# Performance work log

Measured on AMD Instinct MI355X. Metric: run time of the kernel, lower is better.

The kernel has to match this reference:

```python
import jax, jax.numpy as jnp
import numpy as np
from jax import lax

T, B, I, H, C = 256, 64, 256, 512, 64
TOP_K, TRUNC, EPS = 5, 100, 1e-7


def setup_inputs() -> dict:
    key = jax.random.key(0)
    ks = jax.random.split(key, 8)
    s = 1.0 / np.sqrt(H).astype(np.float32)
    return {
        "x": jax.random.normal(ks[0], (T, B, I), jnp.float32),
        "W_ih": jax.random.uniform(ks[1], (4 * H, I), jnp.float32, -s, s),
        "W_hh": jax.random.uniform(ks[2], (4 * H, H), jnp.float32, -s, s),
        "b_ih": jax.random.uniform(ks[3], (4 * H,), jnp.float32, -s, s),
        "b_hh": jax.random.uniform(ks[4], (4 * H,), jnp.float32, -s, s),
        "w_t": jax.random.normal(ks[5], (2 * H, 1), jnp.float32) * 0.01,
        "fc_w": jax.random.normal(ks[6], (C, 2 * H), jnp.float32) * (1.0 / np.sqrt(2.0 * H)),
        "fc_b": jnp.zeros((C,), jnp.float32),
    }


def _forward(x, W_ih, W_hh, b_ih, b_hh, w_t, fc_w, fc_b):
    Tn, Bn, _ = x.shape
    Hn = W_hh.shape[1]
    h0 = jnp.zeros((Bn, Hn), x.dtype)
    c0 = jnp.zeros((Bn, Hn), x.dtype)
    # fixed-size memory buffer; slot 0 holds initial h (zeros), slot i+1 gets h_t of step i
    mem0 = jnp.zeros((Tn, Bn, Hn), x.dtype)
    idx = jnp.arange(Tn)
    wt_vec = w_t[:, 0]

    def step(carry, inp):
        h, c, mem = carry
        x_t, i = inp
        detach = ((i + 1) % TRUNC) == 0  # truncated BPTT boundary
        h_in = jnp.where(detach, lax.stop_gradient(h), h)
        c_in = jnp.where(detach, lax.stop_gradient(c), c)
        gates = x_t @ W_ih.T + b_ih + h_in @ W_hh.T + b_hh  # [B,4H]
        gi, gf, gg, go = jnp.split(gates, 4, axis=1)
        c_new = jax.nn.sigmoid(gf) * c_in + jax.nn.sigmoid(gi) * jnp.tanh(gg)
        h_new = jax.nn.sigmoid(go) * jnp.tanh(c_new)

        valid = (idx <= i)[:, None]  # [T,1]; cur_mem_size = i+1
        feat = jnp.tanh(jnp.concatenate(
            [jnp.broadcast_to(h_new[None], mem.shape), mem], axis=2))  # [T,B,2H]
        scores = jnp.einsum('tbd,d->tb', feat, wt_vec)  # [T,B]
        # top-k threshold over valid memory slots (k-th largest), else min when mem small
        kth = lax.top_k(jnp.where(valid, scores, -jnp.inf).T, TOP_K)[0][:, -1]  # [B]
        mn = jnp.min(jnp.where(valid, scores, jnp.inf), axis=0)  # [B]
        delta = jnp.where(i + 1 <= TOP_K, mn, kth) + EPS
        w = jnp.where(valid, jnp.maximum(scores - delta[None, :], 0.0), 0.0)
        w = w / (jnp.sum(w, axis=0, keepdims=True) + EPS)
        m_t = jnp.einsum('tb,tbh->bh', w, mem)
        h_out = h_new + m_t
        mem = mem.at[i + 1].set(h_out, mode='drop')  # append; OOB at last step dropped
        return (h_out, c_new, mem), (h_out, m_t)

    _, (h_seq, m_seq) = lax.scan(step, (h0, c0, mem0), (x, idx))
    feats = jnp.concatenate([h_seq, m_seq], axis=2)  # [T,B,2H]
    return jnp.einsum('tbd,cd->tbc', feats, fc_w) + fc_b  # [T,B,C]


def reference(x, W_ih, W_hh, b_ih, b_hh, w_t, fc_w, fc_b):
    return _forward(x, W_ih, W_hh, b_ih, b_hh, w_t, fc_w, fc_b)
```

## Files before the change

kernel.cpp:

```cpp
#include <hip/hip_runtime.h>


#define T_N 256
#define B_N 64
#define I_N 256
#define H_N 512
#define C_N 64
#define EPSF 1e-7f

typedef float v4f __attribute__((ext_vector_type(4)));
typedef float v2f __attribute__((ext_vector_type(2)));

#define XT4_F   0u
#define MEM4_F  4194304u
#define MSEQ4_F 12615680u
#define PSUM4_F 21004288u
#define FCWT_F  25214976u
#define FLAG_F  25280512u
#define TOT_F   25280768u

__device__ __forceinline__ float sigf(float x) { return 1.0f / (1.0f + expf(-x)); }

__device__ __forceinline__ void st_lic_f32(float* p, float v) {
  asm volatile("global_store_dword %0, %1, off sc0 sc1" :: "v"(p), "v"(v) : "memory");
}
__device__ __forceinline__ void st_lic_f32x2(float* p, v2f v) {
  asm volatile("global_store_dwordx2 %0, %1, off sc0 sc1" :: "v"(p), "v"(v) : "memory");
}
__device__ __forceinline__ void st_lic_u32(unsigned* p, unsigned v) {
  asm volatile("global_store_dword %0, %1, off sc0 sc1" :: "v"(p), "v"(v) : "memory");
}
__device__ __forceinline__ unsigned ld_lic_u32(const unsigned* p) {
  unsigned r;
  asm volatile("global_load_dword %0, %1, off sc0 sc1\n\ts_waitcnt vmcnt(0)"
               : "=v"(r) : "v"(p) : "memory");
  return r;
}

__device__ __forceinline__ void ins5(float s, int t,
                                     float& v0, float& v1, float& v2, float& v3, float& v4,
                                     int& j0, int& j1, int& j2, int& j3) {
  if (s > v4) {
    if (s > v0)      { v4=v3; v3=v2; j3=j2; v2=v1; j2=j1; v1=v0; j1=j0; v0=s; j0=t; }
    else if (s > v1) { v4=v3; v3=v2; j3=j2; v2=v1; j2=j1; v1=s; j1=t; }
    else if (s > v2) { v4=v3; v3=v2; j3=j2; v2=s; j2=t; }
    else if (s > v3) { v4=v3; v3=s; j3=t; }
    else             { v4=s; }
  }
}

__global__ void poison_k(float* out, int n) {
  int i = blockIdx.x * 256 + threadIdx.x;
  if (i < n) out[i] = __int_as_float(0x7fc00000);
}

__global__ void init_k(const float* __restrict__ x, const float* __restrict__ fc_w,
                       float* __restrict__ ws) {
  __shared__ float tile[64][65];
  const int blk = blockIdx.x, tid = threadIdx.x;
  if (blk < 1024) {
    const int t = blk >> 2, k0 = (blk & 3) * 64;
    for (int u = tid; u < 4096; u += 256) {
      int bb = u >> 6, kk = u & 63;
      tile[kk][bb] = x[((unsigned)t * 64u + bb) * 256u + k0 + kk];
    }
    __syncthreads();
    for (int u = tid; u < 4096; u += 256) {
      int kk = u >> 6, bb = u & 63;
      int k = k0 + kk;
      ws[XT4_F + (unsigned)t * 16384u + (unsigned)(k >> 2) * 256u
         + (unsigned)bb * 4u + (unsigned)(k & 3)] = tile[kk][bb];
    }
  } else {
    const int d0 = (blk - 1024) * 64;
    for (int u = tid; u < 4096; u += 256) {
      int cc = u >> 6, dd = u & 63;
      tile[dd][cc] = fc_w[(unsigned)cc * 1024u + d0 + dd];
    }
    __syncthreads();
    for (int u = tid; u < 4096; u += 256) {
      int dd = u >> 6, cc = u & 63;
      ws[FCWT_F + (unsigned)(d0 + dd) * 64u + cc] = tile[dd][cc];
    }
  }
}

__launch_bounds__(512, 1)
__global__ void lstm_main(const float* __restrict__ W_ih, const float* __restrict__ W_hh,
                          const float* __restrict__ b_ih, const float* __restrict__ b_hh,
                          const float* __restrict__ w_t, float* __restrict__ ws) {
  __shared__ float Wx[I_N][8];
  __shared__ float Wh[H_N][8];
  __shared__ float red2[8][4][B_N][2];
  __shared__ float psum[8][B_N];

  const int g = blockIdx.x;
  const int tid = threadIdx.x;
  const int b = tid & 63;
  const int kqu = __builtin_amdgcn_readfirstlane(tid >> 6);

  unsigned int* flags = (unsigned int*)(ws + FLAG_F);

  for (int idx = tid; idx < 8 * I_N; idx += 512) {
    int rr = idx >> 8, k = idx & (I_N - 1);
    int grow = (rr >> 1) * H_N + 2 * g + (rr & 1);
    Wx[k][rr] = W_ih[grow * I_N + k];
  }
  for (int idx = tid; idx < 8 * H_N; idx += 512) {
    int rr = idx >> 9, k = idx & (H_N - 1);
    int grow = (rr >> 1) * H_N + 2 * g + (rr & 1);
    Wh[k][rr] = W_hh[grow * H_N + k];
  }
  float bias_r[8];
  #pragma unroll
  for (int r = 0; r < 8; ++r) {
    int grow = (r >> 1) * H_N + 2 * g + (r & 1);
    bias_r[r] = b_ih[grow] + b_hh[grow];
  }
  const float wt20 = w_t[H_N + 2 * g];
  const float wt21 = w_t[H_N + 2 * g + 1];
  __syncthreads();

  float cs0 = 0.0f, cs1 = 0.0f;
  float v0 = -3e38f, v1 = -3e38f, v2 = -3e38f, v3 = -3e38f, v4 = -3e38f;
  int j0 = 0, j1 = 0, j2 = 0, j3 = 0;
  float mn = 3e38f;

  const unsigned hoff0 = (unsigned)(g >> 1) * 256u + (unsigned)b * 4u + (unsigned)((g & 1) * 2);

  float xacc[8];
  #pragma unroll
  for (int r = 0; r < 8; ++r) xacc[r] = 0.0f;
  {
    const v4f* xp = (const v4f*)(ws + XT4_F) + (unsigned)(kqu * 8) * 64u + b;
    v4f xv[8];
    #pragma unroll
    for (int j = 0; j < 8; ++j) xv[j] = xp[j * 64];
    #pragma unroll
    for (int j = 0; j < 8; ++j) {
      #pragma unroll
      for (int u = 0; u < 4; ++u) {
        float v = xv[j][u];
        const float* wr = &Wx[kqu * 32 + 4 * j + u][0];
        #pragma unroll
        for (int r = 0; r < 8; ++r) xacc[r] += v * wr[r];
      }
    }
  }

  for (int i = 0; i < T_N; ++i) {
    if (i > 0) {
      const unsigned* fp = flags + (kqu * 32 + (b & 31));
      while (ld_lic_u32(fp) < (unsigned)i) __builtin_amdgcn_s_sleep(1);
    }

    v4f pv[8];
    {
      const v4f* pp = (const v4f*)(ws + PSUM4_F) + (unsigned)i * 4096u
                      + (unsigned)(kqu * 8) * 64u + b;
      #pragma unroll
      for (int j = 0; j < 8; ++j) pv[j] = pp[j * 64];
    }
    v4f hv[16];
    {
      const v4f* hp = (const v4f*)(ws + MEM4_F) + (unsigned)i * 8192u
                      + (unsigned)(kqu * 16) * 64u + b;
      #pragma unroll
      for (int j = 0; j < 16; ++j) hv[j] = hp[j * 64];
    }
    float ps = 0.0f;
    #pragma unroll
    for (int j = 0; j < 8; ++j) ps += (pv[j][0] + pv[j][1]) + (pv[j][2] + pv[j][3]);
    psum[kqu][b] = ps;

    float acc[8];
    #pragma unroll
    for (int r = 0; r < 8; ++r) acc[r] = xacc[r];
    #pragma unroll
    for (int j = 0; j < 16; ++j) {
      #pragma unroll
      for (int u = 0; u < 4; ++u) {
        float v = hv[j][u];
        const float* wr = &Wh[kqu * 64 + 4 * j + u][0];
        #pragma unroll
        for (int r = 0; r < 8; ++r) acc[r] += v * wr[r];
      }
    }
    #pragma unroll
    for (int p = 0; p < 4; ++p) {
      red2[kqu][p][b][0] = acc[2 * p];
      red2[kqu][p][b][1] = acc[2 * p + 1];
    }
    __syncthreads();

    float sc = ((psum[0][b] + psum[1][b]) + (psum[2][b] + psum[3][b]))
             + ((psum[4][b] + psum[5][b]) + (psum[6][b] + psum[7][b]));
    ins5(sc, i, v0, v1, v2, v3, v4, j0, j1, j2, j3);
    mn = fminf(mn, sc);
    float delta = ((i + 1) <= 5 ? mn : v4) + EPSF;
    float w0 = fmaxf(v0 - delta, 0.0f);
    float w1 = fmaxf(v1 - delta, 0.0f);
    float w2 = fmaxf(v2 - delta, 0.0f);
    float w3 = fmaxf(v3 - delta, 0.0f);
    float inv = 1.0f / (w0 + w1 + w2 + w3 + EPSF);
    w0 *= inv; w1 *= inv; w2 *= inv; w3 *= inv;

    const v2f* mb2 = (const v2f*)(ws + MEM4_F + hoff0);
    v2f q0 = mb2[(unsigned)j0 * 16384u];
    v2f q1 = mb2[(unsigned)j1 * 16384u];
    v2f q2 = mb2[(unsigned)j2 * 16384u];
    v2f q3 = mb2[(unsigned)j3 * 16384u];

    float G[8];
    #pragma unroll
    for (int r = 0; r < 8; ++r) G[r] = bias_r[r];
    #pragma unroll
    for (int q = 0; q < 8; ++q) {
      #pragma unroll
      for (int p = 0; p < 4; ++p) {
        G[2 * p]     += red2[q][p][b][0];
        G[2 * p + 1] += red2[q][p][b][1];
      }
    }

    float cn0 = sigf(G[2]) * cs0 + sigf(G[0]) * tanhf(G[4]);
    float hn0 = sigf(G[6]) * tanhf(cn0);
    float cn1 = sigf(G[3]) * cs1 + sigf(G[1]) * tanhf(G[5]);
    float hn1 = sigf(G[7]) * tanhf(cn1);
    cs0 = cn0; cs1 = cn1;

    float m0 = w0 * q0[0] + w1 * q1[0] + w2 * q2[0] + w3 * q3[0];
    float m1 = w0 * q0[1] + w1 * q1[1] + w2 * q2[1] + w3 * q3[1];
    float ho0 = hn0 + m0, ho1 = hn1 + m1;

    if (kqu == 0) {
      v2f hov; hov[0] = ho0; hov[1] = ho1;
      st_lic_f32x2(ws + MEM4_F + (unsigned)(i + 1) * 32768u + hoff0, hov);
    } else if (kqu == 1) {
      v2f mv; mv[0] = m0; mv[1] = m1;
      *(v2f*)(ws + MSEQ4_F + (unsigned)i * 32768u + hoff0) = mv;
    } else if (kqu == 2) {
      st_lic_f32(ws + PSUM4_F + (unsigned)(i + 1) * 16384u + (unsigned)(g >> 2) * 256u
                 + (unsigned)b * 4u + (unsigned)(g & 3),
                 tanhf(ho0) * wt20 + tanhf(ho1) * wt21);
    }
    __syncthreads();
    if (tid == 0) st_lic_u32(&flags[g], (unsigned)(i + 1));

    if (i + 1 < T_N) {
      const v4f* xp = (const v4f*)(ws + XT4_F) + (unsigned)(i + 1) * 4096u
                      + (unsigned)(kqu * 8) * 64u + b;
      v4f xv[8];
      #pragma unroll
      for (int j = 0; j < 8; ++j) xv[j] = xp[j * 64];
      #pragma unroll
      for (int r = 0; r < 8; ++r) xacc[r] = 0.0f;
      #pragma unroll
      for (int j = 0; j < 8; ++j) {
        #pragma unroll
        for (int u = 0; u < 4; ++u) {
          float v = xv[j][u];
          const float* wr = &Wx[kqu * 32 + 4 * j + u][0];
          #pragma unroll
          for (int r = 0; r < 8; ++r) xacc[r] += v * wr[r];
        }
      }
    }
  }
}

__launch_bounds__(256, 4)
__global__ void out_gemm(const float* __restrict__ ws, const float* __restrict__ fc_b,
                         float* __restrict__ out) {
  __shared__ float fw[64][16];
  const int t = blockIdx.x >> 2, cg = blockIdx.x & 3;
  const int tid = threadIdx.x, b = tid & 63, cs = (tid >> 6) * 4;
  float acc[4] = {0.0f, 0.0f, 0.0f, 0.0f};
  const v4f* hsrc = (const v4f*)(ws + MEM4_F) + (unsigned)(t + 1) * 8192u + b;
  const v4f* msrc = (const v4f*)(ws + MSEQ4_F) + (unsigned)t * 8192u + b;
  for (int half = 0; half < 2; ++half) {
    const v4f* src = half ? msrc : hsrc;
    for (int dt = 0; dt < 512; dt += 64) {
      __syncthreads();
      for (int u = tid; u < 1024; u += 256) {
        int dd = u >> 4, cc = u & 15;
        fw[dd][cc] = ws[FCWT_F + (unsigned)(half * 512 + dt + dd) * 64u + cg * 16 + cc];
      }
      __syncthreads();
      #pragma unroll 4
      for (int j = 0; j < 16; ++j) {
        v4f f4 = src[(unsigned)(dt / 4 + j) * 64u];
        #pragma unroll
        for (int u = 0; u < 4; ++u) {
          float f = f4[u];
          const float* wr = &fw[4 * j + u][cs];
          #pragma unroll
          for (int c4 = 0; c4 < 4; ++c4) acc[c4] += f * wr[c4];
        }
      }
    }
  }
  float* op = out + ((unsigned)t * 64u + b) * 64u + cg * 16 + cs;
  #pragma unroll
  for (int c4 = 0; c4 < 4; ++c4) op[c4] = acc[c4] + fc_b[cg * 16 + cs + c4];
}

extern "C" void kernel_launch(void* const* d_in, const int* in_sizes, int n_in,
                              void* d_out, int out_size, void* d_ws, size_t ws_size,
                              hipStream_t stream) {
  const float* x    = (const float*)d_in[0];
  const float* W_ih = (const float*)d_in[1];
  const float* W_hh = (const float*)d_in[2];
  const float* b_ih = (const float*)d_in[3];
  const float* b_hh = (const float*)d_in[4];
  const float* w_t  = (const float*)d_in[5];
  const float* fc_w = (const float*)d_in[6];
  const float* fc_b = (const float*)d_in[7];
  float* out = (float*)d_out;
  float* ws  = (float*)d_ws;

  if (ws_size < (size_t)TOT_F * 4u) {
    poison_k<<<(out_size + 255) / 256, 256, 0, stream>>>(out, out_size);
    return;
  }

  hipMemsetAsync(ws + MEM4_F, 0, (size_t)32768u * 4u, stream);
  hipMemsetAsync(ws + PSUM4_F, 0, (size_t)16384u * 4u, stream);
  hipMemsetAsync(ws + FLAG_F, 0, 256u * 4u, stream);

  init_k<<<1040, 256, 0, stream>>>(x, fc_w, ws);
  lstm_main<<<256, 512, 0, stream>>>(W_ih, W_hh, b_ih, b_hh, w_t, ws);
  out_gemm<<<1024, 256, 0, stream>>>(ws, fc_b, out);
}
```

Before: 1.692 ms.

## Remove second block barrier per step via double-buffered LDS and per-wave flags

Double-buffers the shared reduction arrays by step parity so the trailing __syncthreads can be dropped. Each of two waves now publishes its own completion flag right after its store, and consumers poll both flags with one 64-bit load. The top-k bookkeeping keeps the selected memory values in registers instead of indices, which removes the four gather loads from the memory buffer each step. Only waves 0-2 run the gate and epilogue math, which cuts redundant work but makes correctness depend on the parity buffering and on the cross-block flag ordering.

```diff
diff --git a/kernel.cpp b/kernel.cpp
--- a/kernel.cpp
+++ b/kernel.cpp
@@ -10,6 +10,7 @@
 
 typedef float v4f __attribute__((ext_vector_type(4)));
 typedef float v2f __attribute__((ext_vector_type(2)));
+typedef unsigned v2u __attribute__((ext_vector_type(2)));
 
 #define XT4_F   0u
 #define MEM4_F  4194304u
@@ -17,7 +18,7 @@
 #define PSUM4_F 21004288u
 #define FCWT_F  25214976u
 #define FLAG_F  25280512u
-#define TOT_F   25280768u
+#define TOT_F   25281024u
 
 __device__ __forceinline__ float sigf(float x) { return 1.0f / (1.0f + expf(-x)); }
 
@@ -30,22 +31,31 @@
 __device__ __forceinline__ void st_lic_u32(unsigned* p, unsigned v) {
   asm volatile("global_store_dword %0, %1, off sc0 sc1" :: "v"(p), "v"(v) : "memory");
 }
-__device__ __forceinline__ unsigned ld_lic_u32(const unsigned* p) {
-  unsigned r;
-  asm volatile("global_load_dword %0, %1, off sc0 sc1\n\ts_waitcnt vmcnt(0)"
+__device__ __forceinline__ v2u ld_lic_u32x2(const unsigned* p) {
+  v2u r;
+  asm volatile("global_load_dwordx2 %0, %1, off sc0 sc1\n\ts_waitcnt vmcnt(0)"
                : "=v"(r) : "v"(p) : "memory");
   return r;
 }
 
-__device__ __forceinline__ void ins5(float s, int t,
-                                     float& v0, float& v1, float& v2, float& v3, float& v4,
-                                     int& j0, int& j1, int& j2, int& j3) {
+__device__ __forceinline__ void ins5v(float s, float a0, float a1,
+    float& v0, float& v1, float& v2, float& v3, float& v4,
+    float& qa0, float& qb0, float& qa1, float& qb1,
+    float& qa2, float& qb2, float& qa3, float& qb3) {
   if (s > v4) {
-    if (s > v0)      { v4=v3; v3=v2; j3=j2; v2=v1; j2=j1; v1=v0; j1=j0; v0=s; j0=t; }
-    else if (s > v1) { v4=v3; v3=v2; j3=j2; v2=v1; j2=j1; v1=s; j1=t; }
-    else if (s > v2) { v4=v3; v3=v2; j3=j2; v2=s; j2=t; }
-    else if (s > v3) { v4=v3; v3=s; j3=t; }
-    else             { v4=s; }
+    if (s > v0) {
+      v4=v3; v3=v2; qa3=qa2; qb3=qb2; v2=v1; qa2=qa1; qb2=qb1;
+      v1=v0; qa1=qa0; qb1=qb0; v0=s; qa0=a0; qb0=a1;
+    } else if (s > v1) {
+      v4=v3; v3=v2; qa3=qa2; qb3=qb2; v2=v1; qa2=qa1; qb2=qb1;
+      v1=s; qa1=a0; qb1=a1;
+    } else if (s > v2) {
+      v4=v3; v3=v2; qa3=qa2; qb3=qb2; v2=s; qa2=a0; qb2=a1;
+    } else if (s > v3) {
+      v4=v3; v3=s; qa3=a0; qb3=a1;
+    } else {
+      v4=s;
+    }
   }
 }
 
@@ -91,8 +101,8 @@
                           const float* __restrict__ w_t, float* __restrict__ ws) {
   __shared__ float Wx[I_N][8];
   __shared__ float Wh[H_N][8];
-  __shared__ float red2[8][4][B_N][2];
-  __shared__ float psum[8][B_N];
+  __shared__ float red2[2][8][4][B_N][2];
+  __shared__ float psum[2][8][B_N];
 
   const int g = blockIdx.x;
   const int tid = threadIdx.x;
@@ -122,8 +132,9 @@
   __syncthreads();
 
   float cs0 = 0.0f, cs1 = 0.0f;
+  float po0 = 0.0f, po1 = 0.0f;
   float v0 = -3e38f, v1 = -3e38f, v2 = -3e38f, v3 = -3e38f, v4 = -3e38f;
-  int j0 = 0, j1 = 0, j2 = 0, j3 = 0;
+  float qa0 = 0, qb0 = 0, qa1 = 0, qb1 = 0, qa2 = 0, qb2 = 0, qa3 = 0, qb3 = 0;
   float mn = 3e38f;
 
   const unsigned hoff0 = (unsigned)(g >> 1) * 256u + (unsigned)b * 4u + (unsigned)((g & 1) * 2);
@@ -149,9 +160,15 @@
   }
 
   for (int i = 0; i < T_N; ++i) {
+    const int par = i & 1;
+
     if (i > 0) {
-      const unsigned* fp = flags + (kqu * 32 + (b & 31));
-      while (ld_lic_u32(fp) < (unsigned)i) __builtin_amdgcn_s_sleep(1);
+      const unsigned* fp = flags + 2u * (unsigned)(kqu * 32 + (b & 31));
+      for (;;) {
+        v2u f = ld_lic_u32x2(fp);
+        if (f[0] >= (unsigned)i && f[1] >= (unsigned)i) break;
+        __builtin_amdgcn_s_sleep(1);
+      }
     }
 
     v4f pv[8];
@@ -171,7 +188,7 @@
     float ps = 0.0f;
     #pragma unroll
     for (int j = 0; j < 8; ++j) ps += (pv[j][0] + pv[j][1]) + (pv[j][2] + pv[j][3]);
-    psum[kqu][b] = ps;
+    psum[par][kqu][b] = ps;
 
     float acc[8];
     #pragma unroll
@@ -188,64 +205,64 @@
     }
     #pragma unroll
     for (int p = 0; p < 4; ++p) {
-      red2[kqu][p][b][0] = acc[2 * p];
-      red2[kqu][p][b][1] = acc[2 * p + 1];
+      red2[par][kqu][p][b][0] = acc[2 * p];
+      red2[par][kqu][p][b][1] = acc[2 * p + 1];
     }
     __syncthreads();
 
-    float sc = ((psum[0][b] + psum[1][b]) + (psum[2][b] + psum[3][b]))
-             + ((psum[4][b] + psum[5][b]) + (psum[6][b] + psum[7][b]));
-    ins5(sc, i, v0, v1, v2, v3, v4, j0, j1, j2, j3);
-    mn = fminf(mn, sc);
-    float delta = ((i + 1) <= 5 ? mn : v4) + EPSF;
-    float w0 = fmaxf(v0 - delta, 0.0f);
-    float w1 = fmaxf(v1 - delta, 0.0f);
-    float w2 = fmaxf(v2 - delta, 0.0f);
-    float w3 = fmaxf(v3 - delta, 0.0f);
-    float inv = 1.0f / (w0 + w1 + w2 + w3 + EPSF);
-    w0 *= inv; w1 *= inv; w2 *= inv; w3 *= inv;
-
-    const v2f* mb2 = (const v2f*)(ws + MEM4_F + hoff0);
-    v2f q0 = mb2[(unsigned)j0 * 16384u];
-    v2f q1 = mb2[(unsigned)j1 * 16384u];
-    v2f q2 = mb2[(unsigned)j2 * 16384u];
-    v2f q3 = mb2[(unsigned)j3 * 16384u];
-
-    float G[8];
-    #pragma unroll
-    for (int r = 0; r < 8; ++r) G[r] = bias_r[r];
-    #pragma unroll
-    for (int q = 0; q < 8; ++q) {
-      #pragma unroll
-      for (int p = 0; p < 4; ++p) {
-        G[2 * p]     += red2[q][p][b][0];
-        G[2 * p + 1] += red2[q][p][b][1];
-      }
-    }
-
-    float cn0 = sigf(G[2]) * cs0 + sigf(G[0]) * tanhf(G[4]);
-    float hn0 = sigf(G[6]) * tanhf(cn0);
-    float cn1 = sigf(G[3]) * cs1 + sigf(G[1]) * tanhf(G[5]);
-    float hn1 = sigf(G[7]) * tanhf(cn1);
-    cs0 = cn0; cs1 = cn1;
-
-    float m0 = w0 * q0[0] + w1 * q1[0] + w2 * q2[0] + w3 * q3[0];
-    float m1 = w0 * q0[1] + w1 * q1[1] + w2 * q2[1] + w3 * q3[1];
-    float ho0 = hn0 + m0, ho1 = hn1 + m1;
-
-    if (kqu == 0) {
-      v2f hov; hov[0] = ho0; hov[1] = ho1;
-      st_lic_f32x2(ws + MEM4_F + (unsigned)(i + 1) * 32768u + hoff0, hov);
-    } else if (kqu == 1) {
-      v2f mv; mv[0] = m0; mv[1] = m1;
-      *(v2f*)(ws + MSEQ4_F + (unsigned)i * 32768u + hoff0) = mv;
-    } else if (kqu == 2) {
-      st_lic_f32(ws + PSUM4_F + (unsigned)(i + 1) * 16384u + (unsigned)(g >> 2) * 256u
-                 + (unsigned)b * 4u + (unsigned)(g & 3),
-                 tanhf(ho0) * wt20 + tanhf(ho1) * wt21);
-    }
-    __syncthreads();
-    if (tid == 0) st_lic_u32(&flags[g], (unsigned)(i + 1));
+    if (kqu < 3) {
+      float sc = ((psum[par][0][b] + psum[par][1][b]) + (psum[par][2][b] + psum[par][3][b]))
+               + ((psum[par][4][b] + psum[par][5][b]) + (psum[par][6][b] + psum[par][7][b]));
+      ins5v(sc, po0, po1, v0, v1, v2, v3, v4,
+            qa0, qb0, qa1, qb1, qa2, qb2, qa3, qb3);
+      mn = fminf(mn, sc);
+      float delta = ((i + 1) <= 5 ? mn : v4) + EPSF;
+      float w0 = fmaxf(v0 - delta, 0.0f);
+      float w1 = fmaxf(v1 - delta, 0.0f);
+      float w2 = fmaxf(v2 - delta, 0.0f);
+      float w3 = fmaxf(v3 - delta, 0.0f);
+      float inv = 1.0f / (w0 + w1 + w2 + w3 + EPSF);
+      w0 *= inv; w1 *= inv; w2 *= inv; w3 *= inv;
+
+      float G[8];
+      #pragma unroll
+      for (int r = 0; r < 8; ++r) G[r] = bias_r[r];
+      #pragma unroll
+      for (int q = 0; q < 8; ++q) {
+        #pragma unroll
+        for (int p = 0; p < 4; ++p) {
+          G[2 * p]     += red2[par][q][p][b][0];
+          G[2 * p + 1] += red2[par][q][p][b][1];
+        }
+      }
+
+      float cn0 = sigf(G[2]) * cs0 + sigf(G[0]) * tanhf(G[4]);
+      float hn0 = sigf(G[6]) * tanhf(cn0);
+      float cn1 = sigf(G[3]) * cs1 + sigf(G[1]) * tanhf(G[5]);
+      float hn1 = sigf(G[7]) * tanhf(cn1);
+      cs0 = cn0; cs1 = cn1;
+
+      float m0 = w0 * qa0 + w1 * qa1 + w2 * qa2 + w3 * qa3;
+      float m1 = w0 * qb0 + w1 * qb1 + w2 * qb2 + w3 * qb3;
+      float ho0 = hn0 + m0, ho1 = hn1 + m1;
+      po0 = ho0; po1 = ho1;
+
+      if (kqu == 0) {
+        v2f hov; hov[0] = ho0; hov[1] = ho1;
+        st_lic_f32x2(ws + MEM4_F + (unsigned)(i + 1) * 32768u + hoff0, hov);
+        asm volatile("s_waitcnt vmcnt(0)" ::: "memory");
+        st_lic_u32(&flags[2 * g], (unsigned)(i + 1));
+      } else if (kqu == 1) {
+        v2f mv; mv[0] = m0; mv[1] = m1;
+        *(v2f*)(ws + MSEQ4_F + (unsigned)i * 32768u + hoff0) = mv;
+      } else {
+        st_lic_f32(ws + PSUM4_F + (unsigned)(i + 1) * 16384u + (unsigned)(g >> 2) * 256u
+                   + (unsigned)b * 4u + (unsigned)(g & 3),
+                   tanhf(ho0) * wt20 + tanhf(ho1) * wt21);
+        asm volatile("s_waitcnt vmcnt(0)" ::: "memory");
+        st_lic_u32(&flags[2 * g + 1], (unsigned)(i + 1));
+      }
+    }
 
     if (i + 1 < T_N) {
       const v4f* xp = (const v4f*)(ws + XT4_F) + (unsigned)(i + 1) * 4096u
@@ -326,7 +343,7 @@
 
   hipMemsetAsync(ws + MEM4_F, 0, (size_t)32768u * 4u, stream);
   hipMemsetAsync(ws + PSUM4_F, 0, (size_t)16384u * 4u, stream);
-  hipMemsetAsync(ws + FLAG_F, 0, 256u * 4u, stream);
+  hipMemsetAsync(ws + FLAG_F, 0, 512u * 4u, stream);
 
   init_k<<<1040, 256, 0, stream>>>(x, fc_w, ws);
   lstm_main<<<256, 512, 0, stream>>>(W_ih, W_hh, b_ih, b_hh, w_t, ws);
```

Result: slower. 2.631 ms (+55.5%).
